# Kernel tuning notes

Measured on AMD Instinct MI355X. Metric: run time of the kernel, lower is better.

## Reference

```python
import jax, jax.numpy as jnp
import numpy as np

N_A, N_G, D, H = 100000, 25000, 128, 4
E_B, E_O, E_R, E_P = 400000, 100000, 200000, 200000
BN_INV = float(1.0 / np.sqrt(1.0 + 1e-5))  # eval-mode BatchNorm1d, running mean 0 / var 1


def setup_inputs():
    key = jax.random.key(0)
    ks = iter(jax.random.split(key, 64))
    nrm = lambda shape, s=0.05: jax.random.normal(next(ks), shape, jnp.float32) * s
    ri = lambda n, hi: jax.random.randint(next(ks), (n,), 0, hi, jnp.int32)
    inp = dict(
        x_atom=nrm((N_A, D), 1.0), x_group=nrm((N_G, D), 1.0),
        ef_bond=nrm((E_B, D), 1.0), ef_overlap=nrm((E_O, D), 1.0),
        bond_src=ri(E_B, N_A), bond_dst=ri(E_B, N_A),
        ov_src=ri(E_O, N_G), ov_dst=ri(E_O, N_G),
        ref_src=ri(E_R, N_G), ref_dst=ri(E_R, N_A),
        pool_src=ri(E_P, N_A), pool_dst=ri(E_P, N_G),
    )
    # two GINE convs (bond 'b', overlap 'o'): eps + MLP Linear(D,2D)->BN->ReLU->Linear(2D,D)
    for pre in ('b', 'o'):
        inp[pre + '_eps'] = jnp.zeros((1,), jnp.float32)
        inp[pre + '_W1'] = nrm((D, 2 * D)); inp[pre + '_b1'] = jnp.zeros((2 * D,), jnp.float32)
        inp[pre + '_g1'] = jnp.ones((2 * D,), jnp.float32); inp[pre + '_be1'] = jnp.zeros((2 * D,), jnp.float32)
        inp[pre + '_W2'] = nrm((2 * D, D)); inp[pre + '_b2'] = jnp.zeros((D,), jnp.float32)
    # two ModifiedGATConvs (refine 'r', pool 'p'): GATConv + Flatten->BN->ReLU->Linear
    for pre in ('r', 'p'):
        inp[pre + '_Wfc'] = nrm((D, H * D)); inp[pre + '_al'] = nrm((H, D)); inp[pre + '_ar'] = nrm((H, D))
        inp[pre + '_Wres'] = nrm((D, H * D)); inp[pre + '_bias'] = jnp.zeros((H * D,), jnp.float32)
        inp[pre + '_g'] = jnp.ones((H * D,), jnp.float32); inp[pre + '_b'] = jnp.zeros((H * D,), jnp.float32)
        inp[pre + '_Wout'] = nrm((H * D, D)); inp[pre + '_bout'] = jnp.zeros((D,), jnp.float32)
    return inp


def _gine(x_src, x_dst, efeat, src, dst, n_dst, eps, W1, b1, g1, be1, W2, b2):
    m = jax.nn.relu(x_src[src] + efeat)                       # [E, D] message: relu(h_src + e)
    neigh = jax.ops.segment_sum(m, dst, num_segments=n_dst)   # [Nd, D] sum-reduce
    h = (1.0 + eps) * x_dst + neigh
    h = h @ W1 + b1
    h = jax.nn.relu(g1 * (h * BN_INV) + be1)                  # eval BN
    return h @ W2 + b2


def _gat(x_src, x_dst, src, dst, n_dst, Wfc, al, ar, Wres, bias, g, b, Wout, bout):
    hs = (x_src @ Wfc).reshape(-1, H, D)                      # [Ns, H, D]
    hd = (x_dst @ Wfc).reshape(-1, H, D)
    el = jnp.sum(hs * al, axis=-1)                            # [Ns, H]
    er = jnp.sum(hd * ar, axis=-1)                            # [Nd, H]
    e = jax.nn.leaky_relu(el[src] + er[dst], 0.2)             # [E, H]
    emax = jax.ops.segment_max(e, dst, num_segments=n_dst)    # per-dst softmax (stable)
    ex = jnp.exp(e - emax[dst])
    den = jax.ops.segment_sum(ex, dst, num_segments=n_dst)
    a = ex / jnp.maximum(den[dst], 1e-9)                      # [E, H]
    rst = jax.ops.segment_sum(a[:, :, None] * hs[src], dst, num_segments=n_dst)  # [Nd, H, D]
    rst = rst + (x_dst @ Wres).reshape(-1, H, D) + bias.reshape(H, D)            # residual + bias
    flat = rst.reshape(-1, H * D)                             # Flatten
    h = jax.nn.relu(g * (flat * BN_INV) + b)                  # eval BN -> ReLU
    return h @ Wout + bout


def reference(x_atom, x_group, ef_bond, ef_overlap, bond_src, bond_dst, ov_src, ov_dst, ref_src, ref_dst, pool_src, pool_dst, b_eps, b_W1, b_b1, b_g1, b_be1, b_W2, b_b2, o_eps, o_W1, o_b1, o_g1, o_be1, o_W2, o_b2, r_Wfc, r_al, r_ar, r_Wres, r_bias, r_g, r_b, r_Wout, r_bout, p_Wfc, p_al, p_ar, p_Wres, p_bias, p_g, p_b, p_Wout, p_bout):
    # HeteroGraphConv with default 'sum' cross-relation aggregation per dst node type
    out_atom = _gine(x_atom, x_atom, ef_bond, bond_src, bond_dst, N_A, b_eps, b_W1, b_b1, b_g1, b_be1, b_W2, b_b2)
    out_atom = out_atom + _gat(x_group, x_atom, ref_src, ref_dst, N_A, r_Wfc, r_al, r_ar, r_Wres, r_bias, r_g, r_b, r_Wout, r_bout)
    out_group = _gine(x_group, x_group, ef_overlap, ov_src, ov_dst, N_G, o_eps, o_W1, o_b1, o_g1, o_be1, o_W2, o_b2)
    out_group = out_group + _gat(x_atom, x_group, pool_src, pool_dst, N_G, p_Wfc, p_al, p_ar, p_Wres, p_bias, p_g, p_b, p_Wout, p_bout)
    return jnp.concatenate([out_atom, out_group], axis=0)     # [N_A + N_G, D]
```

## Files before the change

### kernel.cpp

```cpp
#include <hip/hip_runtime.h>
#include <hip/hip_bf16.h>

#define N_A 100000
#define N_G 25000
#define DD 128
#define E_B 400000
#define E_O 100000
#define E_R 200000
#define E_P 200000
#define EALL 900000
#define NSLOT 250000
#define STRIDE 64

static constexpr float BN_INV_C = 0.99999500003749969f;

typedef __attribute__((ext_vector_type(8))) short bf16x8;
typedef __attribute__((ext_vector_type(4))) float f32x4;

__device__ __forceinline__ unsigned short f2bf(float f) {
    unsigned u = __float_as_uint(f);
    unsigned r = (u + 0x7FFFu + ((u >> 16) & 1u)) >> 16;
    return (unsigned short)r;
}
__device__ __forceinline__ float bf2f(unsigned short s) {
    return __uint_as_float(((unsigned)s) << 16);
}
__device__ __forceinline__ float lrelu(float v) { return v > 0.f ? v : 0.2f * v; }

__device__ __forceinline__ void gload16(const unsigned short* g, unsigned short* l) {
    __builtin_amdgcn_global_load_lds(
        (const __attribute__((address_space(1))) void*)g,
        (__attribute__((address_space(3))) void*)l, 16, 0, 0);
}

struct WcSeg { const float* src; unsigned short* dst; int K; int N; int ldk; int off; };
struct PrepArgs {
    const float* xa; const float* xg;
    unsigned short* xab; unsigned short* xgb;
    WcSeg wc[10];
    const float* rWfc; const float* ral; const float* rar;
    const float* pWfc; const float* pal; const float* par;
    float* wv;
    const int* bs; const int* bd; const int* os; const int* od;
    const int* rs; const int* rd; const int* ps; const int* pd;
    int* deg; uint2* adj; int* heads; int* nxt;
};

#define PB_XC 15625
#define PB_WC 2560
#define PB_WAR 8

__global__ __launch_bounds__(256) void k_prep(PrepArgs p) {
    int bx = blockIdx.x, tid = threadIdx.x;
    if (bx < PB_XC) {
        int t = bx * 256 + tid;
        if (t < N_A * 32) {
            float4 v = *(const float4*)(p.xa + (size_t)t * 4);
            ushort4 o; o.x = f2bf(v.x); o.y = f2bf(v.y); o.z = f2bf(v.z); o.w = f2bf(v.w);
            *(ushort4*)(p.xab + (size_t)t * 4) = o;
        } else {
            int t2 = t - N_A * 32;
            if (t2 < N_G * 32) {
                float4 v = *(const float4*)(p.xg + (size_t)t2 * 4);
                ushort4 o; o.x = f2bf(v.x); o.y = f2bf(v.y); o.z = f2bf(v.z); o.w = f2bf(v.w);
                *(ushort4*)(p.xgb + (size_t)t2 * 4) = o;
            }
        }
    } else if (bx < PB_XC + PB_WC) {
        int b2 = bx - PB_XC;
        WcSeg sg = p.wc[b2 >> 8];
        int t = ((b2 & 255) << 8) + tid;
        if (t < sg.K * sg.N) {
            int n = t % sg.N, k = t / sg.N;
            sg.dst[(size_t)n * sg.ldk + sg.off + k] = f2bf(sg.src[t]);
        }
    } else if (bx < PB_XC + PB_WC + PB_WAR) {
        int b3 = bx - (PB_XC + PB_WC);
        int bsel = b3 >> 1;
        int t = ((b3 & 1) << 8) + tid;
        const float* W = bsel < 2 ? p.rWfc : p.pWfc;
        const float* vec = bsel == 0 ? p.ral : bsel == 1 ? p.rar : bsel == 2 ? p.pal : p.par;
        int k = t >> 2, h = t & 3;
        const float* wr = W + (size_t)k * 512 + h * 128;
        const float* av = vec + h * 128;
        float s = 0.f;
        for (int d = 0; d < 128; ++d) s += wr[d] * av[d];
        p.wv[bsel * 512 + t] = s;
    } else {
        int t = (bx - (PB_XC + PB_WC + PB_WAR)) * 256 + tid;
        int e, base, go; const int* S; const int* D;
        if (t < E_B) { e = t; S = p.bs; D = p.bd; base = 0; go = 0; }
        else if (t < E_B + E_O) { e = t - E_B; S = p.os; D = p.od; base = 100000; go = E_B; }
        else if (t < E_B + E_O + E_R) { e = t - (E_B + E_O); S = p.rs; D = p.rd; base = 125000; go = E_B + E_O; }
        else if (t < EALL) { e = t - (E_B + E_O + E_R); S = p.ps; D = p.pd; base = 225000; go = E_B + E_O + E_R; }
        else return;
        int d = D[e], s = S[e];
        int ns = base + d;
        int pos = atomicAdd(&p.deg[ns], 1);
        if (pos < STRIDE) p.adj[(size_t)ns * STRIDE + pos] = make_uint2((unsigned)e, (unsigned)s);
        else p.nxt[go + e] = atomicExch(&p.heads[ns], e);
    }
}

__device__ __forceinline__ void gine_body(
    int bx, int tid,
    const unsigned short* __restrict__ xAb, const unsigned short* __restrict__ xGb,
    const float* __restrict__ efB, const float* __restrict__ efO,
    const int* __restrict__ bsrc, const int* __restrict__ osrc,
    const int* __restrict__ deg, const uint2* __restrict__ adj,
    const int* __restrict__ heads, const int* __restrict__ nxt,
    const float* __restrict__ beps, const float* __restrict__ oeps,
    unsigned short* __restrict__ h0A, unsigned short* __restrict__ h0G,
    uint2* glbuf) {
    int wid = tid >> 6, lane = tid & 63;
    int half = lane >> 5, l32 = lane & 31;
    int n = bx * 4 + wid;
    const unsigned short* xs; const unsigned short* xdrow; const float* ef;
    const int* esrc; const int* nx; float ep; unsigned short* outp; int nn, base;
    if (n < N_A) {
        nn = n; xs = xAb; xdrow = xAb + (size_t)n * DD; ef = efB; esrc = bsrc;
        base = 0; nx = nxt; ep = 1.0f + beps[0]; outp = h0A + (size_t)n * DD;
    } else {
        nn = n - N_A; xs = xGb; xdrow = xGb + (size_t)nn * DD; ef = efO; esrc = osrc;
        base = 100000; nx = nxt + E_B; ep = 1.0f + oeps[0]; outp = h0G + (size_t)nn * DD;
    }
    int d = deg[base + nn];
    int cb = min(d, STRIDE);
    uint2* gl = glbuf + wid * STRIDE;
    if (lane < cb) gl[lane] = adj[(size_t)(base + nn) * STRIDE + lane];
    __syncthreads();
    float4 acc = make_float4(0.f, 0.f, 0.f, 0.f);
    int i = 0;
    for (; i + 4 <= cb; i += 4) {
        uint2 eA = gl[i + half];
        uint2 eB = gl[i + 2 + half];
        uint2 xwA = *(const uint2*)(xs + (size_t)eA.y * DD + l32 * 4);
        float4 evA = *(const float4*)(ef + (size_t)eA.x * DD + l32 * 4);
        uint2 xwB = *(const uint2*)(xs + (size_t)eB.y * DD + l32 * 4);
        float4 evB = *(const float4*)(ef + (size_t)eB.x * DD + l32 * 4);
        acc.x += fmaxf(bf2f((unsigned short)(xwA.x & 0xffff)) + evA.x, 0.f);
        acc.y += fmaxf(bf2f((unsigned short)(xwA.x >> 16)) + evA.y, 0.f);
        acc.z += fmaxf(bf2f((unsigned short)(xwA.y & 0xffff)) + evA.z, 0.f);
        acc.w += fmaxf(bf2f((unsigned short)(xwA.y >> 16)) + evA.w, 0.f);
        acc.x += fmaxf(bf2f((unsigned short)(xwB.x & 0xffff)) + evB.x, 0.f);
        acc.y += fmaxf(bf2f((unsigned short)(xwB.x >> 16)) + evB.y, 0.f);
        acc.z += fmaxf(bf2f((unsigned short)(xwB.y & 0xffff)) + evB.z, 0.f);
        acc.w += fmaxf(bf2f((unsigned short)(xwB.y >> 16)) + evB.w, 0.f);
    }
    for (; i + 2 <= cb; i += 2) {
        uint2 eA = gl[i + half];
        uint2 xwA = *(const uint2*)(xs + (size_t)eA.y * DD + l32 * 4);
        float4 evA = *(const float4*)(ef + (size_t)eA.x * DD + l32 * 4);
        acc.x += fmaxf(bf2f((unsigned short)(xwA.x & 0xffff)) + evA.x, 0.f);
        acc.y += fmaxf(bf2f((unsigned short)(xwA.x >> 16)) + evA.y, 0.f);
        acc.z += fmaxf(bf2f((unsigned short)(xwA.y & 0xffff)) + evA.z, 0.f);
        acc.w += fmaxf(bf2f((unsigned short)(xwA.y >> 16)) + evA.w, 0.f);
    }
    if (i < cb && half == 0) {
        uint2 eA = gl[i];
        uint2 xwA = *(const uint2*)(xs + (size_t)eA.y * DD + l32 * 4);
        float4 evA = *(const float4*)(ef + (size_t)eA.x * DD + l32 * 4);
        acc.x += fmaxf(bf2f((unsigned short)(xwA.x & 0xffff)) + evA.x, 0.f);
        acc.y += fmaxf(bf2f((unsigned short)(xwA.x >> 16)) + evA.y, 0.f);
        acc.z += fmaxf(bf2f((unsigned short)(xwA.y & 0xffff)) + evA.z, 0.f);
        acc.w += fmaxf(bf2f((unsigned short)(xwA.y >> 16)) + evA.w, 0.f);
    }
    if (d > STRIDE && half == 0) {
        for (int e = heads[base + nn]; e >= 0; e = nx[e]) {
            int s = esrc[e];
            uint2 xwA = *(const uint2*)(xs + (size_t)s * DD + l32 * 4);
            float4 evA = *(const float4*)(ef + (size_t)e * DD + l32 * 4);
            acc.x += fmaxf(bf2f((unsigned short)(xwA.x & 0xffff)) + evA.x, 0.f);
            acc.y += fmaxf(bf2f((unsigned short)(xwA.x >> 16)) + evA.y, 0.f);
            acc.z += fmaxf(bf2f((unsigned short)(xwA.y & 0xffff)) + evA.z, 0.f);
            acc.w += fmaxf(bf2f((unsigned short)(xwA.y >> 16)) + evA.w, 0.f);
        }
    }
    acc.x += __shfl_xor(acc.x, 32, 64);
    acc.y += __shfl_xor(acc.y, 32, 64);
    acc.z += __shfl_xor(acc.z, 32, 64);
    acc.w += __shfl_xor(acc.w, 32, 64);
    uint2 xd = *(const uint2*)(xdrow + l32 * 4);
    float r0 = ep * bf2f((unsigned short)(xd.x & 0xffff)) + acc.x;
    float r1 = ep * bf2f((unsigned short)(xd.x >> 16)) + acc.y;
    float r2 = ep * bf2f((unsigned short)(xd.y & 0xffff)) + acc.z;
    float r3 = ep * bf2f((unsigned short)(xd.y >> 16)) + acc.w;
    if (half == 0) {
        uint2 o;
        o.x = (unsigned)f2bf(r0) | ((unsigned)f2bf(r1) << 16);
        o.y = (unsigned)f2bf(r2) | ((unsigned)f2bf(r3) << 16);
        *(uint2*)(outp + l32 * 4) = o;
    }
}

__device__ __forceinline__ void logit_body(
    int t,
    const unsigned short* __restrict__ xAb, const unsigned short* __restrict__ xGb,
    const float* __restrict__ wv,
    float* __restrict__ elR, float* __restrict__ elP,
    float* __restrict__ erR, float* __restrict__ erP) {
    const unsigned short* xr; const float* wl; const float* wr_; float* ol; float* orr; int idx;
    if (t < N_A * 4) {
        idx = t; xr = xAb + (size_t)(t >> 2) * DD; wl = wv + 1024; wr_ = wv + 512;
        ol = elP; orr = erR;
    } else {
        int t2 = t - N_A * 4;
        if (t2 >= N_G * 4) return;
        idx = t2; xr = xGb + (size_t)(t2 >> 2) * DD; wl = wv; wr_ = wv + 1536;
        ol = elR; orr = erP;
    }
    int h = idx & 3;
    float sl = 0.f, sr = 0.f;
#pragma unroll
    for (int k = 0; k < DD; k += 8) {
        uint4 w = *(const uint4*)(xr + k);
        unsigned wa[4] = {w.x, w.y, w.z, w.w};
#pragma unroll
        for (int q = 0; q < 4; ++q) {
            float x0 = bf2f((unsigned short)(wa[q] & 0xffff));
            float x1 = bf2f((unsigned short)(wa[q] >> 16));
            int k0 = (k + q * 2) * 4 + h, k1 = (k + q * 2 + 1) * 4 + h;
            sl += x0 * wl[k0] + x1 * wl[k1];
            sr += x0 * wr_[k0] + x1 * wr_[k1];
        }
    }
    ol[idx] = sl;
    orr[idx] = sr;
}

__global__ __launch_bounds__(256) void k_gather_logit(
    const unsigned short* __restrict__ xAb, const unsigned short* __restrict__ xGb,
    const float* __restrict__ efB, const float* __restrict__ efO,
    const int* __restrict__ bsrc, const int* __restrict__ osrc,
    const int* __restrict__ deg, const uint2* __restrict__ adj,
    const int* __restrict__ heads, const int* __restrict__ nxt,
    const float* __restrict__ beps, const float* __restrict__ oeps,
    unsigned short* __restrict__ h0A, unsigned short* __restrict__ h0G,
    const float* __restrict__ wv,
    float* __restrict__ elR, float* __restrict__ elP,
    float* __restrict__ erR, float* __restrict__ erP) {
    __shared__ uint2 gl[4 * STRIDE];
    int bx = blockIdx.x;
    if (bx < 31250)
        gine_body(bx, threadIdx.x, xAb, xGb, efB, efO, bsrc, osrc, deg, adj, heads, nxt,
                  beps, oeps, h0A, h0G, gl);
    else
        logit_body((bx - 31250) * 256 + threadIdx.x, xAb, xGb, wv, elR, elP, erR, erP);
}

__device__ __forceinline__ void exp_body(
    int t,
    const float* __restrict__ elR, const float* __restrict__ erR,
    const float* __restrict__ elP, const float* __restrict__ erP,
    const int* __restrict__ rs, const int* __restrict__ rd,
    const int* __restrict__ ps, const int* __restrict__ pd,
    float* __restrict__ exR, float* __restrict__ exP,
    float* __restrict__ denR, float* __restrict__ denP) {
    if (t < E_R * 4) {
        int e = t >> 2, h = t & 3;
        float v = lrelu(elR[rs[e] * 4 + h] + erR[rd[e] * 4 + h]);
        float x = __expf(v);
        exR[t] = x;
        atomicAdd(&denR[rd[e] * 4 + h], x);
    } else {
        int t2 = t - E_R * 4;
        if (t2 >= E_P * 4) return;
        int e = t2 >> 2, h = t2 & 3;
        float v = lrelu(elP[ps[e] * 4 + h] + erP[pd[e] * 4 + h]);
        float x = __expf(v);
        exP[t2] = x;
        atomicAdd(&denP[pd[e] * 4 + h], x);
    }
}

__device__ __forceinline__ void att_body(
    int bx, int tid,
    const unsigned short* __restrict__ xAb, const unsigned short* __restrict__ xGb,
    const float* __restrict__ exR, const float* __restrict__ exP,
    const float* __restrict__ denR, const float* __restrict__ denP,
    const int* __restrict__ rsrc, const int* __restrict__ psrc,
    const int* __restrict__ deg, const uint2* __restrict__ adj,
    const int* __restrict__ heads, const int* __restrict__ nxt,
    unsigned short* __restrict__ A2r, unsigned short* __restrict__ A2p,
    uint2* glbuf) {
    int wid = tid >> 6, lane = tid & 63;
    int half = lane >> 5, l32 = lane & 31;
    int n = bx * 4 + wid;
    const unsigned short* xs; const float* ex; const float* den;
    const int* esrc; const int* nx; unsigned short* A2; int nn, base;
    if (n < N_A) {
        nn = n; xs = xGb; ex = exR; den = denR; esrc = rsrc;
        base = 125000; nx = nxt + (E_B + E_O); A2 = A2r + (size_t)n * 512;
    } else {
        nn = n - N_A; xs = xAb; ex = exP; den = denP; esrc = psrc;
        base = 225000; nx = nxt + (E_B + E_O + E_R); A2 = A2p + (size_t)nn * 512;
    }
    int d = deg[base + nn];
    int cb = min(d, STRIDE);
    uint2* gl = glbuf + wid * STRIDE;
    if (lane < cb) gl[lane] = adj[(size_t)(base + nn) * STRIDE + lane];
    __syncthreads();
    float4 dv = *(const float4*)(den + (size_t)nn * 4);
    float inv0 = 1.f / fmaxf(dv.x, 1e-9f);
    float inv1 = 1.f / fmaxf(dv.y, 1e-9f);
    float inv2 = 1.f / fmaxf(dv.z, 1e-9f);
    float inv3 = 1.f / fmaxf(dv.w, 1e-9f);
    float acc[4][4] = {};
    int i = 0;
#define ATT_EDGE(e4_, xw_) { \
        float x0 = bf2f((unsigned short)(xw_.x & 0xffff)); \
        float x1 = bf2f((unsigned short)(xw_.x >> 16)); \
        float x2 = bf2f((unsigned short)(xw_.y & 0xffff)); \
        float x3 = bf2f((unsigned short)(xw_.y >> 16)); \
        float a0 = e4_.x * inv0, a1 = e4_.y * inv1, a2 = e4_.z * inv2, a3 = e4_.w * inv3; \
        acc[0][0] += a0 * x0; acc[0][1] += a0 * x1; acc[0][2] += a0 * x2; acc[0][3] += a0 * x3; \
        acc[1][0] += a1 * x0; acc[1][1] += a1 * x1; acc[1][2] += a1 * x2; acc[1][3] += a1 * x3; \
        acc[2][0] += a2 * x0; acc[2][1] += a2 * x1; acc[2][2] += a2 * x2; acc[2][3] += a2 * x3; \
        acc[3][0] += a3 * x0; acc[3][1] += a3 * x1; acc[3][2] += a3 * x2; acc[3][3] += a3 * x3; }
    for (; i + 4 <= cb; i += 4) {
        uint2 eA = gl[i + half], eB = gl[i + 2 + half];
        float4 e4A = *(const float4*)(ex + (size_t)eA.x * 4);
        uint2 xwA = *(const uint2*)(xs + (size_t)eA.y * DD + l32 * 4);
        float4 e4B = *(const float4*)(ex + (size_t)eB.x * 4);
        uint2 xwB = *(const uint2*)(xs + (size_t)eB.y * DD + l32 * 4);
        ATT_EDGE(e4A, xwA);
        ATT_EDGE(e4B, xwB);
    }
    for (; i + 2 <= cb; i += 2) {
        uint2 eA = gl[i + half];
        float4 e4A = *(const float4*)(ex + (size_t)eA.x * 4);
        uint2 xwA = *(const uint2*)(xs + (size_t)eA.y * DD + l32 * 4);
        ATT_EDGE(e4A, xwA);
    }
    if (i < cb && half == 0) {
        uint2 eA = gl[i];
        float4 e4A = *(const float4*)(ex + (size_t)eA.x * 4);
        uint2 xwA = *(const uint2*)(xs + (size_t)eA.y * DD + l32 * 4);
        ATT_EDGE(e4A, xwA);
    }
    if (d > STRIDE && half == 0) {
        for (int e = heads[base + nn]; e >= 0; e = nx[e]) {
            int s = esrc[e];
            float4 e4A = *(const float4*)(ex + (size_t)e * 4);
            uint2 xwA = *(const uint2*)(xs + (size_t)s * DD + l32 * 4);
            ATT_EDGE(e4A, xwA);
        }
    }
#undef ATT_EDGE
#pragma unroll
    for (int h = 0; h < 4; ++h)
#pragma unroll
        for (int q = 0; q < 4; ++q)
            acc[h][q] += __shfl_xor(acc[h][q], 32, 64);
    if (half == 0) {
#pragma unroll
        for (int h = 0; h < 4; ++h) {
            uint2 o;
            o.x = (unsigned)f2bf(acc[h][0]) | ((unsigned)f2bf(acc[h][1]) << 16);
            o.y = (unsigned)f2bf(acc[h][2]) | ((unsigned)f2bf(acc[h][3]) << 16);
            *(uint2*)(A2 + h * 128 + l32 * 4) = o;
        }
    }
}

template <int EPI, int OUTBF, int GATK>
__device__ __forceinline__ void gemm_body(
    const unsigned short* __restrict__ A, const unsigned short* __restrict__ Bt,
    void* __restrict__ C, int M, int N, int K,
    const float* __restrict__ bias, const float* __restrict__ g,
    const float* __restrict__ be, const unsigned short* __restrict__ addbf,
    const unsigned short* __restrict__ Axd, int bxx, int byy,
    unsigned short* As, unsigned short* Bs) {
    int tid = threadIdx.x;
    int wave = tid >> 6, lane = tid & 63;
    int wr = wave >> 1, wc = wave & 1;
    int row0 = byy * 128, col0 = bxx * 128;
    int l16 = lane & 15, q = lane >> 4;
    int r0s = wave * 16 + (lane >> 2);
    int r1s = r0s + 64;
    int swl = (lane ^ (lane >> 2) ^ (lane >> 4)) & 3;
    int swr = (l16 ^ (l16 >> 2)) & 3;
    unsigned short* ldsA0 = As + wave * 512;
    unsigned short* ldsA1 = As + 2048 + wave * 512;
    unsigned short* ldsB0 = Bs + wave * 512;
    unsigned short* ldsB1 = Bs + 2048 + wave * 512;
    f32x4 acc[4][4] = {};
    for (int k0 = 0; k0 < K; k0 += 32) {
        __syncthreads();
        {
            int kk = k0 + swl * 8;
            int ra0 = min(row0 + r0s, M - 1);
            int ra1 = min(row0 + r1s, M - 1);
            const unsigned short *pa0, *pa1;
            if (GATK) {
                if (k0 < 128) {
                    pa0 = A + (size_t)ra0 * 512 + col0 + kk;
                    pa1 = A + (size_t)ra1 * 512 + col0 + kk;
                } else {
                    pa0 = Axd + (size_t)ra0 * 128 + (kk - 128);
                    pa1 = Axd + (size_t)ra1 * 128 + (kk - 128);
                }
            } else {
                pa0 = A + (size_t)ra0 * K + kk;
                pa1 = A + (size_t)ra1 * K + kk;
            }
            gload16(pa0, ldsA0);
            gload16(pa1, ldsA1);
            gload16(Bt + (size_t)(col0 + r0s) * K + kk, ldsB0);
            gload16(Bt + (size_t)(col0 + r1s) * K + kk, ldsB1);
        }
        __syncthreads();
        bf16x8 af[4], bfr[4];
#pragma unroll
        for (int i = 0; i < 4; ++i) {
            int row = wr * 64 + i * 16 + l16;
            af[i] = *(const bf16x8*)(&As[row * 32 + ((q ^ swr) * 8)]);
        }
#pragma unroll
        for (int j = 0; j < 4; ++j) {
            int row = wc * 64 + j * 16 + l16;
            bfr[j] = *(const bf16x8*)(&Bs[row * 32 + ((q ^ swr) * 8)]);
        }
#pragma unroll
        for (int i = 0; i < 4; ++i)
#pragma unroll
            for (int j = 0; j < 4; ++j)
                acc[i][j] = __builtin_amdgcn_mfma_f32_16x16x32_bf16(af[i], bfr[j], acc[i][j], 0, 0, 0);
    }
    int rq = (lane >> 4) * 4;
#pragma unroll
    for (int i = 0; i < 4; ++i) {
#pragma unroll
        for (int reg = 0; reg < 4; ++reg) {
            int r = row0 + wr * 64 + i * 16 + rq + reg;
            if (r >= M) continue;
#pragma unroll
            for (int j = 0; j < 4; ++j) {
                int c = col0 + wc * 64 + j * 16 + l16;
                float v = acc[i][j][reg];
                size_t idx = (size_t)r * N + c;
                v += bias[c];
                if (EPI == 2) {
                    v = g[c] * (v * BN_INV_C) + be[c];
                    v = fmaxf(v, 0.f);
                }
                if (EPI == 3) {
                    ((float*)C)[idx] = v + bf2f(addbf[idx]);
                } else if (OUTBF) {
                    ((unsigned short*)C)[idx] = f2bf(v);
                } else {
                    ((float*)C)[idx] = v;
                }
            }
        }
    }
}

#define NBA 782
#define NBG 196

__global__ __launch_bounds__(256) void k_gemm1_exp(
    const unsigned short* h0A, const unsigned short* h0G,
    const unsigned short* WtB1, const unsigned short* WtO1,
    const float* bb1, const float* bg1, const float* bbe1,
    const float* ob1, const float* og1, const float* obe1,
    unsigned short* R4a, unsigned short* R4g,
    const float* elR, const float* erR, const float* elP, const float* erP,
    const int* rs, const int* rd, const int* ps, const int* pd,
    float* exR, float* exP, float* denR, float* denP) {
    __shared__ unsigned short As[4096];
    __shared__ unsigned short Bs[4096];
    int b = blockIdx.x;
    if (b < 2 * NBA)
        gemm_body<2, 1, 0>(h0A, WtB1, R4a, N_A, 256, 128, bb1, bg1, bbe1, nullptr, nullptr,
                           b & 1, b >> 1, As, Bs);
    else if (b < 2 * NBA + 2 * NBG) {
        int b2 = b - 2 * NBA;
        gemm_body<2, 1, 0>(h0G, WtO1, R4g, N_G, 256, 128, ob1, og1, obe1, nullptr, nullptr,
                           b2 & 1, b2 >> 1, As, Bs);
    } else {
        int t = (b - (2 * NBA + 2 * NBG)) * 256 + threadIdx.x;
        exp_body(t, elR, erR, elP, erP, rs, rd, ps, pd, exR, exP, denR, denP);
    }
}

__global__ __launch_bounds__(256) void k_att_mid(
    const unsigned short* xAb, const unsigned short* xGb,
    const float* exR, const float* exP, const float* denR, const float* denP,
    const int* rsrc, const int* psrc,
    const int* deg, const uint2* adj, const int* heads, const int* nxt,
    unsigned short* A2r, unsigned short* A2p,
    const unsigned short* R4a, const unsigned short* R4g,
    const unsigned short* WtB2, const unsigned short* WtO2,
    const float* bb2, const float* ob2,
    unsigned short* G1a, unsigned short* G1g) {
    __shared__ unsigned short As[4096];
    __shared__ unsigned short Bs[4096];
    int b = blockIdx.x;
    if (b < 31250)
        att_body(b, threadIdx.x, xAb, xGb, exR, exP, denR, denP, rsrc, psrc,
                 deg, adj, heads, nxt, A2r, A2p, (uint2*)As);
    else if (b < 31250 + NBA)
        gemm_body<1, 1, 0>(R4a, WtB2, G1a, N_A, 128, 256, bb2, nullptr, nullptr, nullptr, nullptr,
                           0, b - 31250, As, Bs);
    else
        gemm_body<1, 1, 0>(R4g, WtO2, G1g, N_G, 128, 256, ob2, nullptr, nullptr, nullptr, nullptr,
                           0, b - 31250 - NBA, As, Bs);
}

__global__ __launch_bounds__(256) void k_gatk(
    const unsigned short* A2r, const unsigned short* A2p,
    const unsigned short* xAb, const unsigned short* xGb,
    const unsigned short* WtR, const unsigned short* WtP,
    const float* rbias, const float* rg, const float* rb,
    const float* pbias, const float* pg, const float* pb,
    unsigned short* R3r, unsigned short* R3p) {
    __shared__ unsigned short As[4096];
    __shared__ unsigned short Bs[4096];
    int b = blockIdx.x;
    if (b < 4 * NBA)
        gemm_body<2, 1, 1>(A2r, WtR, R3r, N_A, 512, 256, rbias, rg, rb, nullptr, xAb,
                           b & 3, b >> 2, As, Bs);
    else {
        int b4 = b - 4 * NBA;
        gemm_body<2, 1, 1>(A2p, WtP, R3p, N_G, 512, 256, pbias, pg, pb, nullptr, xGb,
                           b4 & 3, b4 >> 2, As, Bs);
    }
}

__global__ __launch_bounds__(256) void k_gemm_out(
    const unsigned short* R3r, const unsigned short* R3p,
    const unsigned short* WtRo, const unsigned short* WtPo,
    const float* rbout, const float* pbout,
    const unsigned short* G1a, const unsigned short* G1g,
    float* out) {
    __shared__ unsigned short As[4096];
    __shared__ unsigned short Bs[4096];
    int b = blockIdx.x;
    if (b < NBA)
        gemm_body<3, 0, 0>(R3r, WtRo, out, N_A, 128, 512, rbout, nullptr, nullptr, G1a, nullptr,
                           0, b, As, Bs);
    else
        gemm_body<3, 0, 0>(R3p, WtPo, out + (size_t)N_A * DD, N_G, 128, 512, pbout, nullptr, nullptr,
                           G1g, nullptr, 0, b - NBA, As, Bs);
}

extern "C" void kernel_launch(void* const* d_in, const int* in_sizes, int n_in,
                              void* d_out, int out_size, void* d_ws, size_t ws_size,
                              hipStream_t stream) {
    const float* x_atom = (const float*)d_in[0];
    const float* x_group = (const float*)d_in[1];
    const float* ef_bond = (const float*)d_in[2];
    const float* ef_ov = (const float*)d_in[3];
    const int* bond_src = (const int*)d_in[4];
    const int* bond_dst = (const int*)d_in[5];
    const int* ov_src = (const int*)d_in[6];
    const int* ov_dst = (const int*)d_in[7];
    const int* ref_src = (const int*)d_in[8];
    const int* ref_dst = (const int*)d_in[9];
    const int* pool_src = (const int*)d_in[10];
    const int* pool_dst = (const int*)d_in[11];
    const float* b_eps = (const float*)d_in[12];
    const float* b_W1 = (const float*)d_in[13];
    const float* b_b1 = (const float*)d_in[14];
    const float* b_g1 = (const float*)d_in[15];
    const float* b_be1 = (const float*)d_in[16];
    const float* b_W2 = (const float*)d_in[17];
    const float* b_b2 = (const float*)d_in[18];
    const float* o_eps = (const float*)d_in[19];
    const float* o_W1 = (const float*)d_in[20];
    const float* o_b1 = (const float*)d_in[21];
    const float* o_g1 = (const float*)d_in[22];
    const float* o_be1 = (const float*)d_in[23];
    const float* o_W2 = (const float*)d_in[24];
    const float* o_b2 = (const float*)d_in[25];
    const float* r_Wfc = (const float*)d_in[26];
    const float* r_al = (const float*)d_in[27];
    const float* r_ar = (const float*)d_in[28];
    const float* r_Wres = (const float*)d_in[29];
    const float* r_bias = (const float*)d_in[30];
    const float* r_g = (const float*)d_in[31];
    const float* r_b = (const float*)d_in[32];
    const float* r_Wout = (const float*)d_in[33];
    const float* r_bout = (const float*)d_in[34];
    const float* p_Wfc = (const float*)d_in[35];
    const float* p_al = (const float*)d_in[36];
    const float* p_ar = (const float*)d_in[37];
    const float* p_Wres = (const float*)d_in[38];
    const float* p_bias = (const float*)d_in[39];
    const float* p_g = (const float*)d_in[40];
    const float* p_b = (const float*)d_in[41];
    const float* p_Wout = (const float*)d_in[42];
    const float* p_bout = (const float*)d_in[43];

    float* out = (float*)d_out;
    char* wsb = (char*)d_ws;
    unsigned short* xAb = (unsigned short*)(wsb + 0);
    unsigned short* xGb = (unsigned short*)(wsb + 26000000);
    unsigned short* WtB1 = (unsigned short*)(wsb + 33000000);
    unsigned short* WtB2 = WtB1 + 32768;
    unsigned short* WtO1 = WtB2 + 32768;
    unsigned short* WtO2 = WtO1 + 32768;
    unsigned short* WtR  = WtO2 + 32768;
    unsigned short* WtRo = WtR + 131072;
    unsigned short* WtP  = WtRo + 65536;
    unsigned short* WtPo = WtP + 131072;
    float* wv   = (float*)(wsb + 34100000);
    int* heads  = (int*)(wsb + 36300000);
    int* nxt    = (int*)(wsb + 37400000);
    unsigned short* h0A = (unsigned short*)(wsb + 41100000);
    unsigned short* h0G = (unsigned short*)(wsb + 66800000);
    unsigned short* R4a = (unsigned short*)(wsb + 73300000);
    unsigned short* G1a = (unsigned short*)(wsb + 124600000);
    unsigned short* G1g = (unsigned short*)(wsb + 150300000);
    unsigned short* A2r = (unsigned short*)(wsb + 156800000);
    unsigned short* A2p = (unsigned short*)(wsb + 259300000);
    unsigned short* R3r = (unsigned short*)(wsb + 285000000);
    unsigned short* R3p = (unsigned short*)(wsb + 387500000);
    uint2* adj  = (uint2*)(wsb + 414000000);
    int* deg    = (int*)(wsb + 543000000);
    float* F    = (float*)(wsb + 544000000);
    float* elR  = F;
    float* elP  = F + 100000;
    float* erR  = F + 500000;
    float* erP  = F + 900000;
    float* denR = F + 1000000;
    float* denP = F + 1400000;
    float* exR  = F + 1500000;
    float* exP  = F + 2300000;
    unsigned short* R4g = (unsigned short*)(wsb + 560000000);

    hipMemsetAsync(deg, 0, NSLOT * 4, stream);
    hipMemsetAsync(heads, 0xFF, NSLOT * 4, stream);
    hipMemsetAsync(denR, 0, 500000 * 4, stream);

    PrepArgs pa;
    pa.xa = x_atom; pa.xg = x_group; pa.xab = xAb; pa.xgb = xGb;
    pa.wc[0] = {b_W1, WtB1, 128, 256, 128, 0};
    pa.wc[1] = {b_W2, WtB2, 256, 128, 256, 0};
    pa.wc[2] = {o_W1, WtO1, 128, 256, 128, 0};
    pa.wc[3] = {o_W2, WtO2, 256, 128, 256, 0};
    pa.wc[4] = {r_Wfc, WtR, 128, 512, 256, 0};
    pa.wc[5] = {r_Wres, WtR, 128, 512, 256, 128};
    pa.wc[6] = {r_Wout, WtRo, 512, 128, 512, 0};
    pa.wc[7] = {p_Wfc, WtP, 128, 512, 256, 0};
    pa.wc[8] = {p_Wres, WtP, 128, 512, 256, 128};
    pa.wc[9] = {p_Wout, WtPo, 512, 128, 512, 0};
    pa.rWfc = r_Wfc; pa.ral = r_al; pa.rar = r_ar;
    pa.pWfc = p_Wfc; pa.pal = p_al; pa.par = p_ar; pa.wv = wv;
    pa.bs = bond_src; pa.bd = bond_dst; pa.os = ov_src; pa.od = ov_dst;
    pa.rs = ref_src; pa.rd = ref_dst; pa.ps = pool_src; pa.pd = pool_dst;
    pa.deg = deg; pa.adj = adj; pa.heads = heads; pa.nxt = nxt;
    k_prep<<<PB_XC + PB_WC + PB_WAR + 3516, 256, 0, stream>>>(pa);

    k_gather_logit<<<31250 + 1954, 256, 0, stream>>>(
        xAb, xGb, ef_bond, ef_ov, bond_src, ov_src, deg, adj, heads, nxt,
        b_eps, o_eps, h0A, h0G, wv, elR, elP, erR, erP);

    k_gemm1_exp<<<2 * NBA + 2 * NBG + 6250, 256, 0, stream>>>(
        h0A, h0G, WtB1, WtO1, b_b1, b_g1, b_be1, o_b1, o_g1, o_be1, R4a, R4g,
        elR, erR, elP, erP, ref_src, ref_dst, pool_src, pool_dst, exR, exP, denR, denP);

    k_att_mid<<<31250 + NBA + NBG, 256, 0, stream>>>(
        xAb, xGb, exR, exP, denR, denP, ref_src, pool_src, deg, adj, heads, nxt,
        A2r, A2p, R4a, R4g, WtB2, WtO2, b_b2, o_b2, G1a, G1g);

    k_gatk<<<4 * NBA + 4 * NBG, 256, 0, stream>>>(
        A2r, A2p, xAb, xGb, WtR, WtP,
        r_bias, r_g, r_b, p_bias, p_g, p_b, R3r, R3p);

    k_gemm_out<<<NBA + NBG, 256, 0, stream>>>(R3r, R3p, WtRo, WtPo, r_bout, p_bout,
                                              G1a, G1g, out);
}
```

Baseline: 594.7 us.

## Split attention gather into own kernel, move second GINE GEMM into GAT GEMM launch

Attention aggregation becomes a standalone kernel that uses only a small shared buffer, so it no longer reserves 16 KB of GEMM tile shared memory. This should raise occupancy for the gather-heavy blocks. The second GINE MLP GEMM moves out of that launch and into the GAT fc/residual GEMM launch, so all dense GEMM work of that stage shares one grid. In exchange, the GINE GEMM no longer overlaps with the memory-bound gather.

```diff
diff --git a/kernel.cpp b/kernel.cpp
--- a/kernel.cpp
+++ b/kernel.cpp
@@ -273,19 +273,19 @@
     }
 }
 
-__device__ __forceinline__ void att_body(
-    int bx, int tid,
+__global__ __launch_bounds__(256) void k_att_gather_all(
     const unsigned short* __restrict__ xAb, const unsigned short* __restrict__ xGb,
     const float* __restrict__ exR, const float* __restrict__ exP,
     const float* __restrict__ denR, const float* __restrict__ denP,
     const int* __restrict__ rsrc, const int* __restrict__ psrc,
     const int* __restrict__ deg, const uint2* __restrict__ adj,
     const int* __restrict__ heads, const int* __restrict__ nxt,
-    unsigned short* __restrict__ A2r, unsigned short* __restrict__ A2p,
-    uint2* glbuf) {
+    unsigned short* __restrict__ A2r, unsigned short* __restrict__ A2p) {
+    __shared__ uint2 glbuf[4 * STRIDE];
+    int tid = threadIdx.x;
     int wid = tid >> 6, lane = tid & 63;
     int half = lane >> 5, l32 = lane & 31;
-    int n = bx * 4 + wid;
+    int n = blockIdx.x * 4 + wid;
     const unsigned short* xs; const float* ex; const float* den;
     const int* esrc; const int* nx; unsigned short* A2; int nn, base;
     if (n < N_A) {
@@ -484,31 +484,11 @@
     }
 }
 
-__global__ __launch_bounds__(256) void k_att_mid(
-    const unsigned short* xAb, const unsigned short* xGb,
-    const float* exR, const float* exP, const float* denR, const float* denP,
-    const int* rsrc, const int* psrc,
-    const int* deg, const uint2* adj, const int* heads, const int* nxt,
-    unsigned short* A2r, unsigned short* A2p,
+__global__ __launch_bounds__(256) void k_gatk_mid(
     const unsigned short* R4a, const unsigned short* R4g,
     const unsigned short* WtB2, const unsigned short* WtO2,
     const float* bb2, const float* ob2,
-    unsigned short* G1a, unsigned short* G1g) {
-    __shared__ unsigned short As[4096];
-    __shared__ unsigned short Bs[4096];
-    int b = blockIdx.x;
-    if (b < 31250)
-        att_body(b, threadIdx.x, xAb, xGb, exR, exP, denR, denP, rsrc, psrc,
-                 deg, adj, heads, nxt, A2r, A2p, (uint2*)As);
-    else if (b < 31250 + NBA)
-        gemm_body<1, 1, 0>(R4a, WtB2, G1a, N_A, 128, 256, bb2, nullptr, nullptr, nullptr, nullptr,
-                           0, b - 31250, As, Bs);
-    else
-        gemm_body<1, 1, 0>(R4g, WtO2, G1g, N_G, 128, 256, ob2, nullptr, nullptr, nullptr, nullptr,
-                           0, b - 31250 - NBA, As, Bs);
-}
-
-__global__ __launch_bounds__(256) void k_gatk(
+    unsigned short* G1a, unsigned short* G1g,
     const unsigned short* A2r, const unsigned short* A2p,
     const unsigned short* xAb, const unsigned short* xGb,
     const unsigned short* WtR, const unsigned short* WtP,
@@ -518,11 +498,18 @@
     __shared__ unsigned short As[4096];
     __shared__ unsigned short Bs[4096];
     int b = blockIdx.x;
-    if (b < 4 * NBA)
+    if (b < NBA)
+        gemm_body<1, 1, 0>(R4a, WtB2, G1a, N_A, 128, 256, bb2, nullptr, nullptr, nullptr, nullptr,
+                           0, b, As, Bs);
+    else if (b < NBA + NBG)
+        gemm_body<1, 1, 0>(R4g, WtO2, G1g, N_G, 128, 256, ob2, nullptr, nullptr, nullptr, nullptr,
+                           0, b - NBA, As, Bs);
+    else if (b < NBA + NBG + 4 * NBA) {
+        int b3 = b - (NBA + NBG);
         gemm_body<2, 1, 1>(A2r, WtR, R3r, N_A, 512, 256, rbias, rg, rb, nullptr, xAb,
-                           b & 3, b >> 2, As, Bs);
-    else {
-        int b4 = b - 4 * NBA;
+                           b3 & 3, b3 >> 2, As, Bs);
+    } else {
+        int b4 = b - (NBA + NBG + 4 * NBA);
         gemm_body<2, 1, 1>(A2p, WtP, R3p, N_G, 512, 256, pbias, pg, pb, nullptr, xGb,
                            b4 & 3, b4 >> 2, As, Bs);
     }
@@ -661,11 +648,11 @@
         h0A, h0G, WtB1, WtO1, b_b1, b_g1, b_be1, o_b1, o_g1, o_be1, R4a, R4g,
         elR, erR, elP, erP, ref_src, ref_dst, pool_src, pool_dst, exR, exP, denR, denP);
 
-    k_att_mid<<<31250 + NBA + NBG, 256, 0, stream>>>(
-        xAb, xGb, exR, exP, denR, denP, ref_src, pool_src, deg, adj, heads, nxt,
-        A2r, A2p, R4a, R4g, WtB2, WtO2, b_b2, o_b2, G1a, G1g);
-
-    k_gatk<<<4 * NBA + 4 * NBG, 256, 0, stream>>>(
+    k_att_gather_all<<<31250, 256, 0, stream>>>(
+        xAb, xGb, exR, exP, denR, denP, ref_src, pool_src, deg, adj, heads, nxt, A2r, A2p);
+
+    k_gatk_mid<<<NBA + NBG + 4 * NBA + 4 * NBG, 256, 0, stream>>>(
+        R4a, R4g, WtB2, WtO2, b_b2, o_b2, G1a, G1g,
         A2r, A2p, xAb, xGb, WtR, WtP,
         r_bias, r_g, r_b, p_bias, p_g, p_b, R3r, R3p);
 
```

Result: faster. 527.2 us (-11.3%).
